# Optimization experiments

Measured on AMD Instinct MI355X. Metric: run time of the kernel, lower is better.

The kernel has to match this reference:

```python
import jax, jax.numpy as jnp
import numpy as np

H, L, P, D_MODEL = 8, 4, 4, 256
HD = D_MODEL // H
SPATIAL = np.array([[100, 100], [50, 50], [25, 25], [13, 13]], dtype=np.int64)  # (h, w) per level


def _bilinear_sample(feat, gx, gy, lh, lw):
    """Bilinear sampling matching torch.F.grid_sample(align_corners=False, padding_mode='zeros').
    feat: [BH, lh*lw, D]; gx, gy: [BH, Nq, P] pixel coords. Returns [BH, Nq, P, D]."""
    x0 = jnp.floor(gx); y0 = jnp.floor(gy)
    wx = gx - x0; wy = gy - y0

    def gather(xf, yf):
        xi = xf.astype(jnp.int32); yi = yf.astype(jnp.int32)
        valid = (xi >= 0) & (xi < lw) & (yi >= 0) & (yi < lh)
        idx = jnp.clip(yi, 0, lh - 1) * lw + jnp.clip(xi, 0, lw - 1)
        BH = feat.shape[0]
        v = jnp.take_along_axis(feat, idx.reshape(BH, -1)[:, :, None], axis=1)
        v = v.reshape(xi.shape + (feat.shape[-1],))
        return v * valid[..., None].astype(feat.dtype)

    return (gather(x0, y0) * ((1 - wx) * (1 - wy))[..., None]
            + gather(x0 + 1, y0) * (wx * (1 - wy))[..., None]
            + gather(x0, y0 + 1) * ((1 - wx) * wy)[..., None]
            + gather(x0 + 1, y0 + 1) * (wx * wy)[..., None])


def _msda(query, reference_points, value, sp_np, Wso, bso, Waw, baw, Wv, bv, Wo, bo):
    B, Nq, _ = query.shape
    Nv = value.shape[1]
    v = (value @ Wv + bv).reshape(B, Nv, H, HD)  # value_proj
    off = (query @ Wso + bso).reshape(B, Nq, H, L, P, 2)  # sampling_offsets
    wh = jnp.asarray(sp_np[:, ::-1].copy(), jnp.float32)  # (w, h) per level
    loc = reference_points[:, :, None, :, None, :] + off / wh[None, None, None, :, None, :]
    grid = 2.0 * loc - 1.0  # [B, Nq, H, L, P, 2] in [-1, 1]
    aw = jax.nn.softmax((query @ Waw + baw).reshape(B, Nq, H, L * P), axis=-1).reshape(B, Nq, H, L, P)
    starts = np.concatenate([[0], np.cumsum(sp_np[:, 0] * sp_np[:, 1])]).astype(np.int64)
    out = jnp.zeros((B, H, Nq, HD), dtype=query.dtype)
    for lid in range(L):
        lh, lw = int(sp_np[lid, 0]), int(sp_np[lid, 1])
        feat = v[:, starts[lid]:starts[lid + 1]].transpose(0, 2, 1, 3).reshape(B * H, lh * lw, HD)
        g = grid[:, :, :, lid].transpose(0, 2, 1, 3, 4).reshape(B * H, Nq, P, 2)
        # align_corners=False: x_pix = ((gx + 1) * W - 1) / 2
        gx = (g[..., 0] + 1.0) * (lw * 0.5) - 0.5
        gy = (g[..., 1] + 1.0) * (lh * 0.5) - 0.5
        samp = _bilinear_sample(feat, gx, gy, lh, lw)  # [B*H, Nq, P, HD]
        w_l = aw[:, :, :, lid].transpose(0, 2, 1, 3).reshape(B * H, Nq, P)
        out = out + (samp * w_l[..., None]).sum(axis=2).reshape(B, H, Nq, HD)
    out = out.transpose(0, 2, 1, 3).reshape(B, Nq, D_MODEL)
    return out @ Wo + bo  # output_proj


def setup_inputs() -> dict:
    key = jax.random.key(0)
    ks = jax.random.split(key, 12)
    B, Nq = 2, int(np.sum(SPATIAL[:, 0] * SPATIAL[:, 1]))  # encoder: Nq == Nv == 13294
    Nv = Nq
    s = 1.0 / np.sqrt(D_MODEL).astype(np.float32)
    return {
        "query": jax.random.normal(ks[0], (B, Nq, D_MODEL), jnp.float32),
        "reference_points": jax.random.uniform(ks[1], (B, Nq, L, 2), dtype=jnp.float32),
        "value": jax.random.normal(ks[2], (B, Nv, D_MODEL), jnp.float32),
        "spatial_shapes": jnp.asarray(SPATIAL),
        "Wso": jax.random.normal(ks[3], (D_MODEL, H * L * P * 2), jnp.float32) * 0.01,
        "bso": jax.random.normal(ks[4], (H * L * P * 2,), jnp.float32) * 0.5,
        "Waw": jax.random.normal(ks[5], (D_MODEL, H * L * P), jnp.float32) * 0.01,
        "baw": jnp.zeros((H * L * P,), jnp.float32),
        "Wv": jax.random.normal(ks[6], (D_MODEL, D_MODEL), jnp.float32) * s,
        "bv": jnp.zeros((D_MODEL,), jnp.float32),
        "Wo": jax.random.normal(ks[7], (D_MODEL, D_MODEL), jnp.float32) * s,
        "bo": jnp.zeros((D_MODEL,), jnp.float32),
    }


def reference(query, reference_points, value, spatial_shapes, Wso, bso, Waw, baw, Wv, bv, Wo, bo):
    sp_np = np.asarray(spatial_shapes)  # static level shapes
    return _msda(query, reference_points, value, sp_np, Wso, bso, Waw, baw, Wv, bv, Wo, bo)
```

## Files before the change

### kernel.cpp

```cpp
#include <hip/hip_runtime.h>
#include <hip/hip_bf16.h>
#include <hip/hip_fp16.h>

typedef short s16x8 __attribute__((ext_vector_type(8)));
typedef float f32x4 __attribute__((ext_vector_type(4)));
typedef float f32x2 __attribute__((ext_vector_type(2)));
typedef unsigned int u32x4 __attribute__((ext_vector_type(4)));
typedef unsigned int u32x2 __attribute__((ext_vector_type(2)));

constexpr int Bb = 2, NQ = 13294, Hh = 8, HD = 32;
constexpr int Mrows = Bb * NQ;

__device__ inline short bf16_of(float f) {
  __hip_bfloat16 h = __float2bfloat16(f);
  return *reinterpret_cast<short*>(&h);
}

__global__ __launch_bounds__(256) void prep_k(
    const float* __restrict__ Wv, const float* __restrict__ Wso,
    const float* __restrict__ Waw, const float* __restrict__ Wo,
    const float* __restrict__ bso, const float* __restrict__ baw,
    short* __restrict__ WvT, short* __restrict__ WqT, short* __restrict__ WoT,
    float* __restrict__ bq)
{
  __shared__ short lds[64][65];
  const int tid = threadIdx.x;
  int t = blockIdx.x;
  if (t == 56) {
#pragma unroll
    for (int i = 0; i < 2; i++) {
      int id = i * 256 + tid;
      if (id < 384) bq[id] = id < 256 ? bso[id] : baw[id - 256];
    }
    return;
  }
  const float* src; short* dst; int ldS, n0, k0, drow0;
  if (t < 16)      { src = Wv;  dst = WvT; ldS = 256; n0 = (t >> 2) * 64;        k0 = (t & 3) * 64; drow0 = n0; }
  else if (t < 32) { t -= 16; src = Wso; dst = WqT; ldS = 256; n0 = (t >> 2) * 64; k0 = (t & 3) * 64; drow0 = n0; }
  else if (t < 40) { t -= 32; src = Waw; dst = WqT; ldS = 128; n0 = (t >> 2) * 64; k0 = (t & 3) * 64; drow0 = 256 + n0; }
  else             { t -= 40; src = Wo;  dst = WoT; ldS = 256; n0 = (t >> 2) * 64; k0 = (t & 3) * 64; drow0 = n0; }

#pragma unroll
  for (int i = 0; i < 16; i++) {
    int idx = i * 256 + tid;
    int kk = idx >> 6, nn = idx & 63;
    lds[nn][kk] = bf16_of(src[(size_t)(k0 + kk) * ldS + n0 + nn]);
  }
  __syncthreads();
#pragma unroll
  for (int i = 0; i < 16; i++) {
    int idx = i * 256 + tid;
    int nn = idx >> 6, kk = idx & 63;
    dst[(size_t)(drow0 + nn) * 256 + k0 + kk] = lds[nn][kk];
  }
}

template<int MODE>
__device__ __forceinline__ void gemm_body(
    const void* __restrict__ Araw, const short* __restrict__ WT,
    const float* __restrict__ bias, void* __restrict__ outraw,
    int wg, short (* __restrict__ As)[128][40], short (* __restrict__ Bs)[64][40])
{
  constexpr int NT = (MODE == 1) ? 6 : 4;
  const int xcd = wg & 7, local = wg >> 3;
  const int row0 = (xcd * 26 + local / NT) * 128;
  const int col0 = (local % NT) * 64;
  const int tid = threadIdx.x, lane = tid & 63, wave = tid >> 6;

  f32x4 acc[2][4] = {};

  int arow[2], aq[2], ga[2];
#pragma unroll
  for (int it = 0; it < 2; it++) {
    int task = it * 256 + tid;
    arow[it] = task >> 2; aq[it] = task & 3;
    ga[it] = min(row0 + arow[it], Mrows - 1);
  }
  const int bcol = tid >> 2, bqd = tid & 3;

  f32x4 a0[2], a1[2]; s16x8 abf[2]; s16x8 breg;

  auto load_tile = [&](int kt) {
#pragma unroll
    for (int it = 0; it < 2; it++) {
      if constexpr (MODE == 3) {
        abf[it] = *(const s16x8*)((const short*)Araw + (size_t)ga[it] * 256 + kt + aq[it] * 8);
      } else {
        const float* A = (const float*)Araw;
        a0[it] = *(const f32x4*)(A + (size_t)ga[it] * 256 + kt + aq[it] * 8);
        a1[it] = *(const f32x4*)(A + (size_t)ga[it] * 256 + kt + aq[it] * 8 + 4);
      }
    }
    breg = *(const s16x8*)(WT + (size_t)(col0 + bcol) * 256 + kt + bqd * 8);
  };

  auto write_tile = [&](int buf) {
#pragma unroll
    for (int it = 0; it < 2; it++) {
      s16x8 av;
      if constexpr (MODE == 3) { av = abf[it]; }
      else {
#pragma unroll
        for (int i = 0; i < 4; i++) { av[i] = bf16_of(a0[it][i]); av[4 + i] = bf16_of(a1[it][i]); }
      }
      *(s16x8*)(&As[buf][arow[it]][aq[it] * 8]) = av;
    }
    *(s16x8*)(&Bs[buf][bcol][bqd * 8]) = breg;
  };

  load_tile(0);
  const int fr = lane & 15, kg = lane >> 4;
#pragma unroll
  for (int t = 0; t < 8; t++) {
    const int buf = t & 1;
    write_tile(buf);
    __syncthreads();
    if (t < 7) load_tile((t + 1) * 32);
    s16x8 bfr[4], afr[2];
#pragma unroll
    for (int n = 0; n < 4; n++) bfr[n] = *(const s16x8*)(&Bs[buf][n * 16 + fr][kg * 8]);
#pragma unroll
    for (int m = 0; m < 2; m++) afr[m] = *(const s16x8*)(&As[buf][wave * 32 + m * 16 + fr][kg * 8]);
#pragma unroll
    for (int m = 0; m < 2; m++)
#pragma unroll
      for (int n = 0; n < 4; n++)
        acc[m][n] = __builtin_amdgcn_mfma_f32_16x16x32_bf16(afr[m], bfr[n], acc[m][n], 0, 0, 0);
  }

#pragma unroll
  for (int n = 0; n < 4; n++) {
    const int colL = col0 + n * 16 + fr;
    const float bvf = bias[colL];
#pragma unroll
    for (int m = 0; m < 2; m++) {
#pragma unroll
      for (int r = 0; r < 4; r++) {
        const int rowL = row0 + wave * 32 + m * 16 + kg * 4 + r;
        if (rowL < Mrows) {
          float v = acc[m][n][r] + bvf;
          if constexpr (MODE == 0) {
            int b = rowL >= NQ, nn = rowL - b * NQ;
            int h = colL >> 5, c = colL & 31;
            ((__half*)outraw)[(((size_t)b * Hh + h) * NQ + nn) * HD + c] = __float2half(v);
          } else if constexpr (MODE == 1) {
            ((__hip_bfloat16*)outraw)[(size_t)rowL * 384 + colL] = __float2bfloat16(v);
          } else {
            ((float*)outraw)[(size_t)rowL * 256 + colL] = v;
          }
        }
      }
    }
  }
}

__global__ __launch_bounds__(256) void gemm01_k(
    const float* __restrict__ value, const float* __restrict__ query,
    const short* __restrict__ WvT, const short* __restrict__ WqT,
    const float* __restrict__ bv, const float* __restrict__ bq,
    __half* __restrict__ vproj, __hip_bfloat16* __restrict__ offaw)
{
  __shared__ short As[2][128][40];
  __shared__ short Bs[2][64][40];
  const int wg = blockIdx.x;
  if (wg < 832) gemm_body<0>(value, WvT, bv, vproj, wg, As, Bs);
  else          gemm_body<1>(query, WqT, bq, offaw, wg - 832, As, Bs);
}

__global__ __launch_bounds__(256) void gemm3_k(
    const short* __restrict__ interm, const short* __restrict__ WoT,
    const float* __restrict__ bo, float* __restrict__ out)
{
  __shared__ short As[2][128][40];
  __shared__ short Bs[2][64][40];
  gemm_body<3>(interm, WoT, bo, out, blockIdx.x, As, Bs);
}

__global__ __launch_bounds__(256, 8) void sample_k(
    const __half* __restrict__ vproj,
    const __hip_bfloat16* __restrict__ offaw,
    const float* __restrict__ refp,
    __hip_bfloat16* __restrict__ interm)
{
  __shared__ u32x2 dpk[16][2][65];
  const int plane = blockIdx.x & 15;
  const int chunk = blockIdx.x >> 4;
  const int b = plane >> 3, h = plane & 7;
  const int q0 = chunk * 64;
  const int tid = threadIdx.x;
  const int dims[4]   = {100, 50, 25, 13};
  const int starts[4] = {0, 10000, 12500, 13125};

#pragma unroll
  for (int it = 0; it < 4; it++) {
    const int task = it * 256 + tid;
    const int ql = task >> 4, lp = task & 15;
    const int l = lp >> 2;
    const int lw = dims[l];
    int q = q0 + ql; if (q >= NQ) q = NQ - 1;
    const size_t row = (size_t)b * NQ + q;
    unsigned int oxy = *(const unsigned int*)((const unsigned short*)offaw + row * 384 + h * 32 + lp * 2);
    float offx = __uint_as_float(oxy << 16);
    float offy = __uint_as_float(oxy & 0xffff0000u);
    float logit = __bfloat162float(offaw[row * 384 + 256 + h * 16 + lp]);
    float2 rp = *(const float2*)(refp + (row * 4 + l) * 2);
    float gx = rp.x * (float)lw + offx - 0.5f;
    float gy = rp.y * (float)lw + offy - 0.5f;
    float mx = logit;
#pragma unroll
    for (int d = 1; d < 16; d <<= 1) mx = fmaxf(mx, __shfl_xor(mx, d));
    float e = __expf(logit - mx);
    float ssum = e;
#pragma unroll
    for (int d = 1; d < 16; d <<= 1) ssum += __shfl_xor(ssum, d);
    float aw = e / ssum;

    float xf = floorf(gx), yf = floorf(gy);
    int x0 = (int)xf, y0 = (int)yf;
    float wx = gx - xf, wy = gy - yf;
    int bx = min(max(x0, 0), lw - 2);
    bool lxv = (x0 >= 0) & (x0 < lw);
    bool rxv = (x0 + 1 >= 0) & (x0 + 1 < lw);
    float wl = 1.f - wx, wr = wx;
    float ws0 = (lxv && x0 == bx     ? wl : 0.f) + (rxv && x0 + 1 == bx     ? wr : 0.f);
    float ws1 = (lxv && x0 == bx + 1 ? wl : 0.f) + (rxv && x0 + 1 == bx + 1 ? wr : 0.f);
    const int pbase = (b * Hh + h) * NQ + starts[l];
#pragma unroll
    for (int yi = 0; yi < 2; yi++) {
      int yc = y0 + yi;
      bool yv = (yc >= 0) & (yc < lw);
      int ycl = min(max(yc, 0), lw - 1);
      float wyt = (yi ? wy : 1.f - wy) * aw * (yv ? 1.f : 0.f);
      __half h0 = __float2half(ws0 * wyt);
      __half h1 = __float2half(ws1 * wyt);
      u32x2 pk;
      pk[0] = (unsigned int)((pbase + ycl * lw + bx) << 6);
      pk[1] = (unsigned int)(*(unsigned short*)&h0)
            | ((unsigned int)(*(unsigned short*)&h1) << 16);
      dpk[lp][yi][ql] = pk;
    }
  }
  __syncthreads();

  const int wv = tid >> 6, lane = tid & 63;
  const int qsub = lane >> 2, c = lane & 3;
  const int ql = wv * 16 + qsub;
  const char* vpc = (const char*)vproj + c * 16;
  __half2 accA[4] = {};
  __half2 accB[4] = {};
#pragma unroll 4
  for (int lp = 0; lp < 16; lp++) {
#pragma unroll
    for (int yi = 0; yi < 2; yi++) {
      const u32x2 d = dpk[lp][yi][ql];
      const char* p = vpc + d[0];
      const u32x4 u0 = *(const u32x4*)p;
      const u32x4 u1 = *(const u32x4*)(p + 64);
      unsigned int dw = d[1];
      __half2 hw = *reinterpret_cast<__half2*>(&dw);
      __half2 w00 = __half2half2(__low2half(hw));
      __half2 w11 = __half2half2(__high2half(hw));
#pragma unroll
      for (int j = 0; j < 4; j++) {
        unsigned int t0 = u0[j], t1 = u1[j];
        __half2 v0 = *reinterpret_cast<__half2*>(&t0);
        __half2 v1 = *reinterpret_cast<__half2*>(&t1);
        accA[j] = __hfma2(v0, w00, accA[j]);
        accB[j] = __hfma2(v1, w11, accB[j]);
      }
    }
  }
  const int q = q0 + ql;
  if (q < NQ) {
    unsigned int up[4];
#pragma unroll
    for (int j = 0; j < 4; j++) {
      float2 fa = __half22float2(accA[j]);
      float2 fb = __half22float2(accB[j]);
      unsigned int b0 = (unsigned int)(unsigned short)bf16_of(fa.x + fb.x);
      unsigned int b1 = (unsigned int)(unsigned short)bf16_of(fa.y + fb.y);
      up[j] = (b1 << 16) | b0;
    }
    u32x4 pk = { up[0], up[1], up[2], up[3] };
    *(u32x4*)((unsigned short*)interm + ((size_t)b * NQ + q) * 256 + h * 32 + c * 8) = pk;
  }
}

extern "C" void kernel_launch(void* const* d_in, const int* in_sizes, int n_in,
                              void* d_out, int out_size, void* d_ws, size_t ws_size,
                              hipStream_t stream)
{
  const float* query = (const float*)d_in[0];
  const float* refp  = (const float*)d_in[1];
  const float* value = (const float*)d_in[2];
  const float* Wso = (const float*)d_in[4];
  const float* bso = (const float*)d_in[5];
  const float* Waw = (const float*)d_in[6];
  const float* baw = (const float*)d_in[7];
  const float* Wv  = (const float*)d_in[8];
  const float* bv  = (const float*)d_in[9];
  const float* Wo  = (const float*)d_in[10];
  const float* bo  = (const float*)d_in[11];

  char* ws = (char*)d_ws;
  __half* vproj          = (__half*)ws;
  __hip_bfloat16* offaw  = (__hip_bfloat16*)(ws + 13613056);
  __hip_bfloat16* interm = (__hip_bfloat16*)(ws + 34032640);
  short* WvT = (short*)(ws + 47645696);
  short* WqT = (short*)(ws + 47776768);
  short* WoT = (short*)(ws + 47973376);
  float* bq  = (float*)(ws + 48104448);
  float* out = (float*)d_out;

  dim3 blk(256);
  prep_k<<<dim3(57), blk, 0, stream>>>(Wv, Wso, Waw, Wo, bso, baw, WvT, WqT, WoT, bq);
  gemm01_k<<<dim3(832 + 1248), blk, 0, stream>>>(value, query, WvT, WqT, bv, bq, vproj, offaw);
  sample_k<<<dim3(16 * 208), blk, 0, stream>>>(vproj, offaw, refp, interm);
  gemm3_k<<<dim3(832), blk, 0, stream>>>((const short*)interm, WoT, bo, out);
}
```

Baseline: 97.90 us.

## Fuse deformable sampling with output projection GEMM via shared-memory tile

```diff
diff --git a/kernel.cpp b/kernel.cpp
--- a/kernel.cpp
+++ b/kernel.cpp
@@ -78,19 +78,14 @@
   }
   const int bcol = tid >> 2, bqd = tid & 3;
 
-  f32x4 a0[2], a1[2]; s16x8 abf[2]; s16x8 breg;
+  f32x4 a0[2], a1[2]; s16x8 breg;
 
   auto load_tile = [&](int kt) {
-#pragma unroll
-    for (int it = 0; it < 2; it++) {
-      if constexpr (MODE == 3) {
-        abf[it] = *(const s16x8*)((const short*)Araw + (size_t)ga[it] * 256 + kt + aq[it] * 8);
-      } else {
-        const float* A = (const float*)Araw;
-        a0[it] = *(const f32x4*)(A + (size_t)ga[it] * 256 + kt + aq[it] * 8);
-        a1[it] = *(const f32x4*)(A + (size_t)ga[it] * 256 + kt + aq[it] * 8 + 4);
-      }
-    }
+    const float* A = (const float*)Araw;
+    a0[0] = *(const f32x4*)(A + (size_t)ga[0] * 256 + kt + aq[0] * 8);
+    a1[0] = *(const f32x4*)(A + (size_t)ga[0] * 256 + kt + aq[0] * 8 + 4);
+    a0[1] = *(const f32x4*)(A + (size_t)ga[1] * 256 + kt + aq[1] * 8);
+    a1[1] = *(const f32x4*)(A + (size_t)ga[1] * 256 + kt + aq[1] * 8 + 4);
     breg = *(const s16x8*)(WT + (size_t)(col0 + bcol) * 256 + kt + bqd * 8);
   };
 
@@ -98,11 +93,8 @@
 #pragma unroll
     for (int it = 0; it < 2; it++) {
       s16x8 av;
-      if constexpr (MODE == 3) { av = abf[it]; }
-      else {
-#pragma unroll
-        for (int i = 0; i < 4; i++) { av[i] = bf16_of(a0[it][i]); av[4 + i] = bf16_of(a1[it][i]); }
-      }
+#pragma unroll
+      for (int i = 0; i < 4; i++) { av[i] = bf16_of(a0[it][i]); av[4 + i] = bf16_of(a1[it][i]); }
       *(s16x8*)(&As[buf][arow[it]][aq[it] * 8]) = av;
     }
     *(s16x8*)(&Bs[buf][bcol][bqd * 8]) = breg;
@@ -143,10 +135,8 @@
             int b = rowL >= NQ, nn = rowL - b * NQ;
             int h = colL >> 5, c = colL & 31;
             ((__half*)outraw)[(((size_t)b * Hh + h) * NQ + nn) * HD + c] = __float2half(v);
-          } else if constexpr (MODE == 1) {
+          } else {
             ((__hip_bfloat16*)outraw)[(size_t)rowL * 384 + colL] = __float2bfloat16(v);
-          } else {
-            ((float*)outraw)[(size_t)rowL * 256 + colL] = v;
           }
         }
       }
@@ -167,122 +157,148 @@
   else          gemm_body<1>(query, WqT, bq, offaw, wg - 832, As, Bs);
 }
 
-__global__ __launch_bounds__(256) void gemm3_k(
-    const short* __restrict__ interm, const short* __restrict__ WoT,
-    const float* __restrict__ bo, float* __restrict__ out)
-{
-  __shared__ short As[2][128][40];
-  __shared__ short Bs[2][64][40];
-  gemm_body<3>(interm, WoT, bo, out, blockIdx.x, As, Bs);
-}
-
-__global__ __launch_bounds__(256, 8) void sample_k(
+__global__ __launch_bounds__(256, 3) void sample_o_k(
     const __half* __restrict__ vproj,
     const __hip_bfloat16* __restrict__ offaw,
     const float* __restrict__ refp,
-    __hip_bfloat16* __restrict__ interm)
+    const short* __restrict__ WoT,
+    const float* __restrict__ bo,
+    float* __restrict__ out)
 {
   __shared__ u32x2 dpk[16][2][65];
-  const int plane = blockIdx.x & 15;
-  const int chunk = blockIdx.x >> 4;
-  const int b = plane >> 3, h = plane & 7;
-  const int q0 = chunk * 64;
+  __shared__ short sI[64][264];
+  const int q0 = blockIdx.x * 64;
   const int tid = threadIdx.x;
+  const int wv = tid >> 6, lane = tid & 63;
   const int dims[4]   = {100, 50, 25, 13};
   const int starts[4] = {0, 10000, 12500, 13125};
 
-#pragma unroll
-  for (int it = 0; it < 4; it++) {
-    const int task = it * 256 + tid;
-    const int ql = task >> 4, lp = task & 15;
-    const int l = lp >> 2;
-    const int lw = dims[l];
-    int q = q0 + ql; if (q >= NQ) q = NQ - 1;
-    const size_t row = (size_t)b * NQ + q;
-    unsigned int oxy = *(const unsigned int*)((const unsigned short*)offaw + row * 384 + h * 32 + lp * 2);
-    float offx = __uint_as_float(oxy << 16);
-    float offy = __uint_as_float(oxy & 0xffff0000u);
-    float logit = __bfloat162float(offaw[row * 384 + 256 + h * 16 + lp]);
-    float2 rp = *(const float2*)(refp + (row * 4 + l) * 2);
-    float gx = rp.x * (float)lw + offx - 0.5f;
-    float gy = rp.y * (float)lw + offy - 0.5f;
-    float mx = logit;
-#pragma unroll
-    for (int d = 1; d < 16; d <<= 1) mx = fmaxf(mx, __shfl_xor(mx, d));
-    float e = __expf(logit - mx);
-    float ssum = e;
-#pragma unroll
-    for (int d = 1; d < 16; d <<= 1) ssum += __shfl_xor(ssum, d);
-    float aw = e / ssum;
-
-    float xf = floorf(gx), yf = floorf(gy);
-    int x0 = (int)xf, y0 = (int)yf;
-    float wx = gx - xf, wy = gy - yf;
-    int bx = min(max(x0, 0), lw - 2);
-    bool lxv = (x0 >= 0) & (x0 < lw);
-    bool rxv = (x0 + 1 >= 0) & (x0 + 1 < lw);
-    float wl = 1.f - wx, wr = wx;
-    float ws0 = (lxv && x0 == bx     ? wl : 0.f) + (rxv && x0 + 1 == bx     ? wr : 0.f);
-    float ws1 = (lxv && x0 == bx + 1 ? wl : 0.f) + (rxv && x0 + 1 == bx + 1 ? wr : 0.f);
-    const int pbase = (b * Hh + h) * NQ + starts[l];
-#pragma unroll
-    for (int yi = 0; yi < 2; yi++) {
-      int yc = y0 + yi;
-      bool yv = (yc >= 0) & (yc < lw);
-      int ycl = min(max(yc, 0), lw - 1);
-      float wyt = (yi ? wy : 1.f - wy) * aw * (yv ? 1.f : 0.f);
-      __half h0 = __float2half(ws0 * wyt);
-      __half h1 = __float2half(ws1 * wyt);
-      u32x2 pk;
-      pk[0] = (unsigned int)((pbase + ycl * lw + bx) << 6);
-      pk[1] = (unsigned int)(*(unsigned short*)&h0)
-            | ((unsigned int)(*(unsigned short*)&h1) << 16);
-      dpk[lp][yi][ql] = pk;
-    }
-  }
-  __syncthreads();
-
-  const int wv = tid >> 6, lane = tid & 63;
-  const int qsub = lane >> 2, c = lane & 3;
-  const int ql = wv * 16 + qsub;
-  const char* vpc = (const char*)vproj + c * 16;
-  __half2 accA[4] = {};
-  __half2 accB[4] = {};
+#pragma unroll 1
+  for (int h = 0; h < 8; h++) {
+#pragma unroll
+    for (int it = 0; it < 4; it++) {
+      const int task = it * 256 + tid;
+      const int ql = task >> 4, lp = task & 15;
+      const int l = lp >> 2;
+      const int lw = dims[l];
+      int qg = q0 + ql; if (qg >= Mrows) qg = Mrows - 1;
+      const int b = qg >= NQ;
+      const size_t row = (size_t)qg;
+      unsigned int oxy = *(const unsigned int*)((const unsigned short*)offaw + row * 384 + h * 32 + lp * 2);
+      float offx = __uint_as_float(oxy << 16);
+      float offy = __uint_as_float(oxy & 0xffff0000u);
+      float logit = __bfloat162float(offaw[row * 384 + 256 + h * 16 + lp]);
+      float2 rp = *(const float2*)(refp + (row * 4 + l) * 2);
+      float gx = rp.x * (float)lw + offx - 0.5f;
+      float gy = rp.y * (float)lw + offy - 0.5f;
+      float mx = logit;
+#pragma unroll
+      for (int d = 1; d < 16; d <<= 1) mx = fmaxf(mx, __shfl_xor(mx, d));
+      float e = __expf(logit - mx);
+      float ssum = e;
+#pragma unroll
+      for (int d = 1; d < 16; d <<= 1) ssum += __shfl_xor(ssum, d);
+      float aw = e / ssum;
+
+      float xf = floorf(gx), yf = floorf(gy);
+      int x0 = (int)xf, y0 = (int)yf;
+      float wx = gx - xf, wy = gy - yf;
+      int bx = min(max(x0, 0), lw - 2);
+      bool lxv = (x0 >= 0) & (x0 < lw);
+      bool rxv = (x0 + 1 >= 0) & (x0 + 1 < lw);
+      float wl = 1.f - wx, wr = wx;
+      float ws0 = (lxv && x0 == bx     ? wl : 0.f) + (rxv && x0 + 1 == bx     ? wr : 0.f);
+      float ws1 = (lxv && x0 == bx + 1 ? wl : 0.f) + (rxv && x0 + 1 == bx + 1 ? wr : 0.f);
+      const int pbase = (b * Hh + h) * NQ + starts[l];
+#pragma unroll
+      for (int yi = 0; yi < 2; yi++) {
+        int yc = y0 + yi;
+        bool yv = (yc >= 0) & (yc < lw);
+        int ycl = min(max(yc, 0), lw - 1);
+        float wyt = (yi ? wy : 1.f - wy) * aw * (yv ? 1.f : 0.f);
+        __half h0 = __float2half(ws0 * wyt);
+        __half h1 = __float2half(ws1 * wyt);
+        u32x2 pk;
+        pk[0] = (unsigned int)((pbase + ycl * lw + bx) << 6);
+        pk[1] = (unsigned int)(*(unsigned short*)&h0)
+              | ((unsigned int)(*(unsigned short*)&h1) << 16);
+        dpk[lp][yi][ql] = pk;
+      }
+    }
+    __syncthreads();
+
+    {
+      const int qsub = lane >> 2, c = lane & 3;
+      const int ql = wv * 16 + qsub;
+      const char* vpc = (const char*)vproj + c * 16;
+      __half2 accA[4] = {};
+      __half2 accB[4] = {};
 #pragma unroll 4
-  for (int lp = 0; lp < 16; lp++) {
-#pragma unroll
-    for (int yi = 0; yi < 2; yi++) {
-      const u32x2 d = dpk[lp][yi][ql];
-      const char* p = vpc + d[0];
-      const u32x4 u0 = *(const u32x4*)p;
-      const u32x4 u1 = *(const u32x4*)(p + 64);
-      unsigned int dw = d[1];
-      __half2 hw = *reinterpret_cast<__half2*>(&dw);
-      __half2 w00 = __half2half2(__low2half(hw));
-      __half2 w11 = __half2half2(__high2half(hw));
+      for (int lp = 0; lp < 16; lp++) {
+#pragma unroll
+        for (int yi = 0; yi < 2; yi++) {
+          const u32x2 d = dpk[lp][yi][ql];
+          const char* p = vpc + d[0];
+          const u32x4 u0 = *(const u32x4*)p;
+          const u32x4 u1 = *(const u32x4*)(p + 64);
+          unsigned int dw = d[1];
+          __half2 hw = *reinterpret_cast<__half2*>(&dw);
+          __half2 w00 = __half2half2(__low2half(hw));
+          __half2 w11 = __half2half2(__high2half(hw));
+#pragma unroll
+          for (int j = 0; j < 4; j++) {
+            unsigned int t0 = u0[j], t1 = u1[j];
+            __half2 v0 = *reinterpret_cast<__half2*>(&t0);
+            __half2 v1 = *reinterpret_cast<__half2*>(&t1);
+            accA[j] = __hfma2(v0, w00, accA[j]);
+            accB[j] = __hfma2(v1, w11, accB[j]);
+          }
+        }
+      }
+      unsigned int up[4];
 #pragma unroll
       for (int j = 0; j < 4; j++) {
-        unsigned int t0 = u0[j], t1 = u1[j];
-        __half2 v0 = *reinterpret_cast<__half2*>(&t0);
-        __half2 v1 = *reinterpret_cast<__half2*>(&t1);
-        accA[j] = __hfma2(v0, w00, accA[j]);
-        accB[j] = __hfma2(v1, w11, accB[j]);
-      }
-    }
-  }
-  const int q = q0 + ql;
-  if (q < NQ) {
-    unsigned int up[4];
-#pragma unroll
-    for (int j = 0; j < 4; j++) {
-      float2 fa = __half22float2(accA[j]);
-      float2 fb = __half22float2(accB[j]);
-      unsigned int b0 = (unsigned int)(unsigned short)bf16_of(fa.x + fb.x);
-      unsigned int b1 = (unsigned int)(unsigned short)bf16_of(fa.y + fb.y);
-      up[j] = (b1 << 16) | b0;
-    }
-    u32x4 pk = { up[0], up[1], up[2], up[3] };
-    *(u32x4*)((unsigned short*)interm + ((size_t)b * NQ + q) * 256 + h * 32 + c * 8) = pk;
+        float2 fa = __half22float2(accA[j]);
+        float2 fb = __half22float2(accB[j]);
+        unsigned int b0 = (unsigned int)(unsigned short)bf16_of(fa.x + fb.x);
+        unsigned int b1 = (unsigned int)(unsigned short)bf16_of(fa.y + fb.y);
+        up[j] = (b1 << 16) | b0;
+      }
+      u32x4 pk = { up[0], up[1], up[2], up[3] };
+      *(u32x4*)((char*)&sI[ql][0] + h * 64 + c * 16) = pk;
+    }
+    __syncthreads();
+  }
+
+  const int fr = lane & 15, kg = lane >> 4;
+  f32x4 acc[4][4] = {};
+#pragma unroll
+  for (int kt = 0; kt < 256; kt += 32) {
+    s16x8 afr[4], bfr[4];
+#pragma unroll
+    for (int m = 0; m < 4; m++)
+      afr[m] = *(const s16x8*)((const char*)&sI[m * 16 + fr][0] + (kt + kg * 8) * 2);
+#pragma unroll
+    for (int n = 0; n < 4; n++)
+      bfr[n] = *(const s16x8*)(WoT + (size_t)(wv * 64 + n * 16 + fr) * 256 + kt + kg * 8);
+#pragma unroll
+    for (int m = 0; m < 4; m++)
+#pragma unroll
+      for (int n = 0; n < 4; n++)
+        acc[m][n] = __builtin_amdgcn_mfma_f32_16x16x32_bf16(afr[m], bfr[n], acc[m][n], 0, 0, 0);
+  }
+#pragma unroll
+  for (int n = 0; n < 4; n++) {
+    const int colL = wv * 64 + n * 16 + fr;
+    const float bvf = bo[colL];
+#pragma unroll
+    for (int m = 0; m < 4; m++) {
+#pragma unroll
+      for (int r = 0; r < 4; r++) {
+        const int rowG = q0 + m * 16 + kg * 4 + r;
+        if (rowG < Mrows) out[(size_t)rowG * 256 + colL] = acc[m][n][r] + bvf;
+      }
+    }
   }
 }
 
@@ -305,7 +321,6 @@
   char* ws = (char*)d_ws;
   __half* vproj          = (__half*)ws;
   __hip_bfloat16* offaw  = (__hip_bfloat16*)(ws + 13613056);
-  __hip_bfloat16* interm = (__hip_bfloat16*)(ws + 34032640);
   short* WvT = (short*)(ws + 47645696);
   short* WqT = (short*)(ws + 47776768);
   short* WoT = (short*)(ws + 47973376);
@@ -315,6 +330,5 @@
   dim3 blk(256);
   prep_k<<<dim3(57), blk, 0, stream>>>(Wv, Wso, Waw, Wo, bso, baw, WvT, WqT, WoT, bq);
   gemm01_k<<<dim3(832 + 1248), blk, 0, stream>>>(value, query, WvT, WqT, bv, bq, vproj, offaw);
-  sample_k<<<dim3(16 * 208), blk, 0, stream>>>(vproj, offaw, refp, interm);
-  gemm3_k<<<dim3(832), blk, 0, stream>>>((const short*)interm, WoT, bo, out);
-}
+  sample_o_k<<<dim3(416), blk, 0, stream>>>(vproj, offaw, refp, WoT, bo, out);
+}
```

Measured after the change: 105.4 us. 1.08x slower.
